# Kernel optimization log

Measured on AMD Instinct MI355X. Metric: run time of the kernel, lower is better.

## Reference

```python
import jax, jax.numpy as jnp
import numpy as np

N = 65536      # voxels
NFIX = 4096    # fixed-BC voxels (x == 0)
H = 128        # MLP hidden width
NFORCE = 4096  # force-surface points
E0 = 1.0
NU = 0.3
PENAL = 3.0
EM_V = 1e-3    # element volume
L_FIX = 0.05   # BC ramp length for analytical fixed-BC scale
K_FIX = E0 * 100.0
NUM_HUTCH = 50


def mlp(params, x):
    W1, b1, W2, b2, W3, b3, W4, b4 = params
    h = jnp.tanh(x @ W1 + b1)
    h = jnp.tanh(h @ W2 + b2)
    h = jnp.tanh(h @ W3 + b3)
    return h @ W4 + b4


def bc_scale(coord):
    # analytical fixed-BC scale: 0 exactly on the fixed face (x==0), ramps to 1
    return jnp.clip(coord[..., 0] / L_FIX, 0.0, 1.0)


def hutchinson_trace(params, coords, key, num_samples=NUM_HUTCH):
    # tr(J J^T) estimate via v^T J J^T v = ||J^T v||^2, batched VJPs (replaces
    # the per-sample autograd.grad python loop).
    out, vjp_fn = jax.vjp(lambda p: mlp(p, coords), params)

    def step(acc, k):
        v = jax.random.normal(k, out.shape, dtype=out.dtype)
        (g,) = vjp_fn(v)
        flat = jnp.concatenate([x.reshape(-1) for x in jax.tree_util.tree_leaves(g)])
        return acc + flat @ flat, None

    keys = jax.random.split(key, num_samples)
    tot, _ = jax.lax.scan(step, jnp.float32(0.0), keys)
    return tot / num_samples


def setup_inputs() -> dict:
    key = jax.random.key(0)
    ks = jax.random.split(key, 12)
    coord = jax.random.uniform(ks[0], (N, 3), dtype=jnp.float32)
    coord = coord.at[:, 0].set(0.02 + 0.98 * coord[:, 0])  # free voxels: x > 0
    coord = coord.at[:NFIX, 0].set(0.0)                    # fixed voxels: x == 0
    xPhys_m = jax.random.uniform(ks[1], (N, 1), dtype=jnp.float32)
    def lin(k, fi, fo):
        return jax.random.normal(k, (fi, fo), dtype=jnp.float32) / jnp.sqrt(jnp.float32(fi))
    W1 = lin(ks[2], 3, H); b1 = jnp.zeros((H,), jnp.float32)
    W2 = lin(ks[3], H, H); b2 = jnp.zeros((H,), jnp.float32)
    W3 = lin(ks[4], H, H); b3 = jnp.zeros((H,), jnp.float32)
    W4 = lin(ks[5], H, 3); b4 = jnp.zeros((3,), jnp.float32)
    force_coords = jax.random.uniform(ks[6], (NFORCE, 3), dtype=jnp.float32)
    F_vector = jax.random.normal(ks[7], (3,), dtype=jnp.float32)
    return dict(xPhys_m=xPhys_m, coord=coord, W1=W1, b1=b1, W2=W2, b2=b2,
                W3=W3, b3=b3, W4=W4, b4=b4, force_coords=force_coords,
                F_vector=F_vector, n_fix=NFIX)


def reference(xPhys_m, coord, W1, b1, W2, b2, W3, b3, W4, b4,
              force_coords, F_vector, n_fix):
    params = (W1, b1, W2, b2, W3, b3, W4, b4)

    u = mlp(params, coord)                       # [N,3] displacements
    scale = bc_scale(coord)                      # [N]
    fixed_mask = (scale == 0.0)

    # fixed-BC penalty energy
    u_fix = u * fixed_mask[:, None].astype(u.dtype)
    E_fix_all = xPhys_m ** PENAL * 0.5 * K_FIX * jnp.sum(u_fix ** 2, axis=1, keepdims=True)
    n_fix_ratio = jnp.float32(n_fix) / jnp.float32(N)
    E_fix = jnp.mean(E_fix_all[:n_fix]) * n_fix_ratio * EM_V

    # NTK-based adaptive weight via Hutchinson trace (detached, like .item())
    hkey = jax.random.key(42)
    ku, kr = jax.random.split(hkey)
    tr_uu = hutchinson_trace(params, coord[:n_fix], ku)
    tr_rr = hutchinson_trace(params, coord[n_fix:], kr)
    lam_fix = jax.lax.stop_gradient(jnp.clip(tr_rr / (tr_uu + 1e-12), 1e-3, 1e3))

    # per-voxel displacement Jacobian J[n, i, j] = d u_i / d coord_j  (batched
    # fwd-mode replaces three autograd.grad calls)
    J = jax.vmap(jax.jacfwd(lambda c: mlp(params, c)))(coord)  # [N,3,3]
    ux = J[:, 1, :]   # grads of u[:,1] (u0 in source)
    uy = J[:, 0, :]   # grads of u[:,0] (u1 in source)
    uz = J[:, 2, :]
    eps11 = ux[:, 1]
    eps12 = 0.5 * ux[:, 0] + 0.5 * uy[:, 1]
    eps13 = 0.5 * ux[:, 2] + 0.5 * uz[:, 1]
    eps22 = uy[:, 0]
    eps23 = 0.5 * uy[:, 2] + 0.5 * uz[:, 0]
    eps33 = uz[:, 2]

    lame_mu = E0 / (2.0 * (1.0 + NU))
    lame_lambda = E0 * NU / ((1.0 + NU) * (1.0 - 2.0 * NU))
    tr_strain = eps11 + eps22 + eps33
    sq_diag = eps11 * eps11 + eps22 * eps22 + eps33 * eps33
    energy = (0.5 * lame_lambda * tr_strain * tr_strain
              + lame_mu * (sq_diag + 2.0 * (eps12 * eps12 + eps13 * eps13 + eps23 * eps23)))
    energy = energy[:, None] * xPhys_m ** PENAL   # [N,1]
    energy_c = energy * 2.0
    energy_ans = EM_V * jnp.mean(energy)

    force_l = jnp.sum(mlp(params, force_coords) @ F_vector)

    loss = energy_ans - force_l + lam_fix * E_fix
    return (loss, energy_c, u)
```

## Files before the change

### kernel.cpp

```cpp
#include <hip/hip_runtime.h>
#include <math.h>

typedef __bf16 bf16x8 __attribute__((ext_vector_type(8)));
typedef __bf16 bf16x4 __attribute__((ext_vector_type(4)));
typedef float f32x4 __attribute__((ext_vector_type(4)));

#define HDIM 128
#define NTHREADS 512

#define EMV 0.001f
#define LFIX 0.05f
#define KFIX 100.0f
#define LAMBDA_L 0.5769230769230769f
#define MU_L 0.3846153846153846f

__device__ __forceinline__ int swb(int r, int blk) {
    return (r << 7) + ((blk ^ (r & 7)) << 3);
}
__device__ __forceinline__ int swb32(int r, int g) {
    return (r << 5) + ((g ^ ((r >> 1) & 3)) << 3);
}

__device__ __forceinline__ float fast_tanh(float x) {
    float xc = fminf(fmaxf(x, -10.f), 10.f);
    float e = __expf(2.f * xc);
    return 1.f - 2.f * __builtin_amdgcn_rcpf(e + 1.f);
}

__device__ __forceinline__ float wred(float v) {
#pragma unroll
    for (int off = 32; off > 0; off >>= 1) v += __shfl_down(v, off, 64);
    return v;
}

template <int NB, int CT0, int CT1>
__device__ __forceinline__ void gemm_f8(const bf16x8 (&aw)[4],
                                        __bf16* const* inb, __bf16* const* outb,
                                        const float* __restrict__ bsL,
                                        int wid, int l15, int q) {
    f32x4 acc[NB][CT1 - CT0];
#pragma unroll
    for (int b = 0; b < NB; ++b)
#pragma unroll
        for (int c = 0; c < CT1 - CT0; ++c) acc[b][c] = (f32x4){0.f, 0.f, 0.f, 0.f};

#pragma unroll
    for (int s = 0; s < 4; ++s)
#pragma unroll
        for (int b = 0; b < NB; ++b)
#pragma unroll
            for (int c = CT0; c < CT1; ++c) {
                bf16x8 bfr = *(const bf16x8*)(inb[b] + swb(c * 16 + l15, s * 4 + q));
                acc[b][c - CT0] = __builtin_amdgcn_mfma_f32_16x16x32_bf16(
                    aw[s], bfr, acc[b][c - CT0], 0, 0, 0);
            }
    __syncthreads();
    const int n0 = wid * 16 + q * 4;
    float4 bv = *(const float4*)(bsL + n0);
    float bias4[4] = {bv.x, bv.y, bv.z, bv.w};
#pragma unroll
    for (int c = CT0; c < CT1; ++c) {
        const int p = c * 16 + l15;
        const int widx = swb(p, n0 >> 3) + (n0 & 7);
        bf16x4 hv;
        float fct[4];
#pragma unroll
        for (int i = 0; i < 4; ++i) {
            float h = fast_tanh(acc[0][c - CT0][i] + bias4[i]);
            hv[i] = (__bf16)h;
            fct[i] = 1.f - h * h;
        }
        *(bf16x4*)(outb[0] + widx) = hv;
#pragma unroll
        for (int b = 1; b < NB; ++b) {
            bf16x4 ov;
#pragma unroll
            for (int i = 0; i < 4; ++i) ov[i] = (__bf16)(acc[b][c - CT0][i] * fct[i]);
            *(bf16x4*)(outb[b] + widx) = ov;
        }
    }
}

template <int NB>
__device__ __forceinline__ void gemm_tr8(const float* __restrict__ Wg, __bf16* Wst,
                                         __bf16* const* bufs,
                                         const __bf16* __restrict__ href,
                                         int wid, int l15, int q, int tid) {
    f32x4 acc[NB][2];
#pragma unroll
    for (int b = 0; b < NB; ++b) {
        acc[b][0] = (f32x4){0.f, 0.f, 0.f, 0.f};
        acc[b][1] = (f32x4){0.f, 0.f, 0.f, 0.f};
    }
#pragma unroll
    for (int c = 0; c < 4; ++c) {
        __syncthreads();
        {
            int j = tid >> 2, k8 = tid & 3;
            const float4* src = (const float4*)(Wg + j * HDIM + c * 32 + k8 * 8);
            float4 v0 = src[0], v1 = src[1];
            bf16x8 pk = {(__bf16)v0.x, (__bf16)v0.y, (__bf16)v0.z, (__bf16)v0.w,
                         (__bf16)v1.x, (__bf16)v1.y, (__bf16)v1.z, (__bf16)v1.w};
            *(bf16x8*)(Wst + swb32(j, k8)) = pk;
        }
        __syncthreads();
        bf16x8 afr = *(const bf16x8*)(Wst + swb32(wid * 16 + l15, q));
#pragma unroll
        for (int b = 0; b < NB; ++b) {
            bf16x8 b0 = *(const bf16x8*)(bufs[b] + swb(l15, c * 4 + q));
            acc[b][0] = __builtin_amdgcn_mfma_f32_16x16x32_bf16(afr, b0, acc[b][0], 0, 0, 0);
            bf16x8 b1 = *(const bf16x8*)(bufs[b] + swb(16 + l15, c * 4 + q));
            acc[b][1] = __builtin_amdgcn_mfma_f32_16x16x32_bf16(afr, b1, acc[b][1], 0, 0, 0);
        }
    }
    __syncthreads();
    const int n0 = wid * 16 + q * 4;
#pragma unroll
    for (int ct = 0; ct < 2; ++ct) {
        const int p = ct * 16 + l15;
        const int widx = swb(p, n0 >> 3) + (n0 & 7);
        bf16x4 hv = *(const bf16x4*)(href + widx);
        float fct[4];
#pragma unroll
        for (int i = 0; i < 4; ++i) {
            float h = (float)hv[i];
            fct[i] = 1.f - h * h;
        }
#pragma unroll
        for (int b = 0; b < NB; ++b) {
            bf16x4 ov;
#pragma unroll
            for (int i = 0; i < 4; ++i) ov[i] = (__bf16)(acc[b][ct][i] * fct[i]);
            *(bf16x4*)(bufs[b] + widx) = ov;
        }
    }
}

__device__ __forceinline__ void dnorms8(const __bf16* a, const __bf16* b, const __bf16* c2,
                                        float* npart, int tid) {
    int p = tid & 31, cc = tid >> 5;
    bf16x8 v0 = *(const bf16x8*)(a + swb(p, cc));
    bf16x8 v1 = *(const bf16x8*)(b + swb(p, cc));
    bf16x8 v2 = *(const bf16x8*)(c2 + swb(p, cc));
    float s0 = 0.f, s1 = 0.f, s2 = 0.f;
#pragma unroll
    for (int e = 0; e < 8; ++e) {
        float f0 = (float)v0[e], f1 = (float)v1[e], f2 = (float)v2[e];
        s0 += f0 * f0;
        s1 += f1 * f1;
        s2 += f2 * f2;
    }
    npart[(0 + cc) * 32 + p] = s0;
    npart[(16 + cc) * 32 + p] = s1;
    npart[(32 + cc) * 32 + p] = s2;
}

__device__ __forceinline__ float sum16(const float* npart, int buf, int p) {
    float d = 0.f;
#pragma unroll
    for (int i = 0; i < 16; ++i) d += npart[(buf * 16 + i) * 32 + p];
    return d;
}
__device__ __forceinline__ float sum48(const float* npart, int p) {
    float d = 0.f;
#pragma unroll
    for (int i = 0; i < 48; ++i) d += npart[i * 32 + p];
    return d;
}

__global__ void __launch_bounds__(NTHREADS, 4) pinn_all(
    const float* __restrict__ xPhys, const float* __restrict__ coord,
    const float* __restrict__ W1, const float* __restrict__ b1,
    const float* __restrict__ W2, const float* __restrict__ b2,
    const float* __restrict__ W3, const float* __restrict__ b3,
    const float* __restrict__ W4, const float* __restrict__ b4,
    const float* __restrict__ fc, const float* __restrict__ Fv,
    const int* __restrict__ nfixp,
    float* __restrict__ energy_c_out, float* __restrict__ u_out,
    float* __restrict__ acc, int nm32, int nmain64, int ntrb, int NF) {
    __shared__ __align__(16) __bf16 pool[32768];
    __shared__ __align__(16) __bf16 W4p[16 * HDIM];
    __shared__ __align__(16) float W1s[4 * HDIM];
    __shared__ __align__(16) float W4ts[3 * HDIM];
    __shared__ __align__(16) float gls[64 * 12];
    __shared__ __align__(16) float uls[64 * 4];
    __shared__ float nh1s[32], nh2s[32], nh3s[32];

    const int tid = threadIdx.x;
    const int lane = tid & 63, wid = tid >> 6, l15 = lane & 15, q = lane >> 4;
    const int bi = blockIdx.x;
    const int nfixv = nfixp[0];

    int ttile = -1;
    if (bi < ntrb) {
        const int nfull = nfixv >> 5;
        const int cm = (nfixv & 31) ? 1 : 0;
        const int c1 = (nfull + 7) >> 3;
        int t;
        if (bi < c1) {
            t = bi << 3;
        } else if (cm && bi == c1) {
            t = nfull;
        } else {
            const int rr0 = nfull + cm;
            const int f0 = rr0 + ((8 - (rr0 & 15) + 16) & 15);
            t = f0 + ((bi - c1 - cm) << 4);
        }
        if (t >= nm32) return;
        ttile = t;
    }

    for (int i = tid; i < 3 * HDIM; i += NTHREADS) W1s[i] = W1[i];
    if (tid < HDIM) W1s[3 * HDIM + tid] = b1[tid];
    if (tid < 3 * HDIM) W4ts[tid] = W4[(tid & 127) * 3 + (tid >> 7)];
    if (tid < 256) {
        int o = tid >> 4, blk = tid & 15, j0 = blk * 8;
        bf16x8 pk;
#pragma unroll
        for (int e = 0; e < 8; ++e) pk[e] = (__bf16)((o < 3) ? W4[(j0 + e) * 3 + o] : 0.f);
        *(bf16x8*)(W4p + swb(o, blk)) = pk;
    }
    bf16x8 aw2[4], aw3[4];
#pragma unroll
    for (int s = 0; s < 4; ++s) {
        const int kb = s * 32 + q * 8;
        const int n = wid * 16 + l15;
        bf16x8 v2, v3;
#pragma unroll
        for (int e = 0; e < 8; ++e) {
            v2[e] = (__bf16)W2[(kb + e) * HDIM + n];
            v3[e] = (__bf16)W3[(kb + e) * HDIM + n];
        }
        aw2[s] = v2;
        aw3[s] = v3;
    }
    __syncthreads();

    if (bi < ntrb) {
        const int base = ttile * 32;
        __bf16* H1 = pool;
        __bf16* H2 = pool + 4096;
        __bf16* H3 = pool + 8192;
        __bf16* T0 = pool + 12288;
        __bf16* T1 = pool + 16384;
        __bf16* T2 = pool + 20480;
        __bf16* WST = pool + 24576;
        float* npart = (float*)(pool + 28672);

        {
            const int p = lane & 31, sub = lane >> 5;
            const int blk = wid * 2 + sub, j0 = blk * 8;
            const float* cp = coord + (base + p) * 3;
            float x0 = cp[0], x1 = cp[1], x2 = cp[2];
            bf16x8 hv, t0v, t1v, t2v;
#pragma unroll
            for (int jj = 0; jj < 8; ++jj) {
                int j = j0 + jj;
                float w0 = W1s[j], w1 = W1s[HDIM + j], w2 = W1s[2 * HDIM + j];
                float z = W1s[3 * HDIM + j] + x0 * w0 + x1 * w1 + x2 * w2;
                float h = fast_tanh(z);
                float fct = 1.f - h * h;
                hv[jj] = (__bf16)h;
                t0v[jj] = (__bf16)(fct * w0);
                t1v[jj] = (__bf16)(fct * w1);
                t2v[jj] = (__bf16)(fct * w2);
            }
            int wi = swb(p, blk);
            *(bf16x8*)(H1 + wi) = hv;
            *(bf16x8*)(T0 + wi) = t0v;
            *(bf16x8*)(T1 + wi) = t1v;
            *(bf16x8*)(T2 + wi) = t2v;
        }
        __syncthreads();
        {
            __bf16* ib[4] = {H1, T0, T1, T2};
            __bf16* ob[4] = {H2, T0, T1, T2};
            gemm_f8<4, 0, 2>(aw2, ib, ob, b2, wid, l15, q);
        }
        __syncthreads();
        {
            __bf16* ib[4] = {H2, T0, T1, T2};
            __bf16* ob[4] = {H3, T0, T1, T2};
            gemm_f8<4, 0, 2>(aw3, ib, ob, b3, wid, l15, q);
        }
        __syncthreads();

        dnorms8(H1, H2, H3, npart, tid);
        __syncthreads();
        if (tid < 32) {
            nh1s[tid] = sum16(npart, 0, tid);
            nh2s[tid] = sum16(npart, 1, tid);
            nh3s[tid] = sum16(npart, 2, tid);
        }
        __syncthreads();
        {
            const int p = lane & 31, sub = lane >> 5;
            const int blk = wid * 2 + sub, j0 = blk * 8;
            bf16x8 h3v = *(const bf16x8*)(H3 + swb(p, blk));
            bf16x8 d0, d1, d2;
#pragma unroll
            for (int e = 0; e < 8; ++e) {
                float h = (float)h3v[e];
                float fct = 1.f - h * h;
                d0[e] = (__bf16)(fct * W4ts[j0 + e]);
                d1[e] = (__bf16)(fct * W4ts[HDIM + j0 + e]);
                d2[e] = (__bf16)(fct * W4ts[2 * HDIM + j0 + e]);
            }
            int wi = swb(p, blk);
            *(bf16x8*)(T0 + wi) = d0;
            *(bf16x8*)(T1 + wi) = d1;
            *(bf16x8*)(T2 + wi) = d2;
        }
        __syncthreads();
        float s_acc = 0.f;
        dnorms8(T0, T1, T2, npart, tid);
        __syncthreads();
        if (tid < 32) s_acc = sum48(npart, tid) * (1.f + nh2s[tid]);
        {
            __bf16* ib[3] = {T0, T1, T2};
            gemm_tr8<3>(W3, WST, ib, H2, wid, l15, q, tid);
        }
        __syncthreads();
        dnorms8(T0, T1, T2, npart, tid);
        __syncthreads();
        if (tid < 32) s_acc += sum48(npart, tid) * (1.f + nh1s[tid]);
        {
            __bf16* ib[3] = {T0, T1, T2};
            gemm_tr8<3>(W2, WST, ib, H1, wid, l15, q, tid);
        }
        __syncthreads();
        dnorms8(T0, T1, T2, npart, tid);
        __syncthreads();
        if (tid < 64) {
            float su = 0.f, sr = 0.f, cu = 0.f, cr = 0.f;
            if (tid < 32) {
                int p = tid;
                const float* cp = coord + (base + p) * 3;
                float x0 = cp[0], x1 = cp[1], x2 = cp[2];
                float nx = x0 * x0 + x1 * x1 + x2 * x2;
                float s = s_acc + sum48(npart, p) * (1.f + nx) + 3.f * (nh3s[p] + 1.f);
                bool uu = (base + p) < nfixv;
                su = uu ? s : 0.f;
                sr = uu ? 0.f : s;
                cu = uu ? 1.f : 0.f;
                cr = uu ? 0.f : 1.f;
            }
            su = wred(su);
            sr = wred(sr);
            cu = wred(cu);
            cr = wred(cr);
            if (tid == 0) {
                atomicAdd(acc + 3, su);
                atomicAdd(acc + 4, sr);
                atomicAdd(acc + 5, cu);
                atomicAdd(acc + 6, cr);
            }
        }
    } else if (bi < ntrb + nmain64) {
        const int base = (bi - ntrb) * 64;
        __bf16* HF = pool;
        __bf16* TF0 = pool + 8192;
        __bf16* TF1 = pool + 16384;
        __bf16* TF2 = pool + 24576;

        {
            const int p = lane;
            const float* cp = coord + (base + p) * 3;
            float x0 = cp[0], x1 = cp[1], x2 = cp[2];
#pragma unroll
            for (int it2 = 0; it2 < 2; ++it2) {
                const int blk = it2 * 8 + wid, j0 = blk * 8;
                bf16x8 hv, t0v, t1v, t2v;
#pragma unroll
                for (int jj = 0; jj < 8; ++jj) {
                    int j = j0 + jj;
                    float w0 = W1s[j], w1 = W1s[HDIM + j], w2 = W1s[2 * HDIM + j];
                    float z = W1s[3 * HDIM + j] + x0 * w0 + x1 * w1 + x2 * w2;
                    float h = fast_tanh(z);
                    float fct = 1.f - h * h;
                    hv[jj] = (__bf16)h;
                    t0v[jj] = (__bf16)(fct * w0);
                    t1v[jj] = (__bf16)(fct * w1);
                    t2v[jj] = (__bf16)(fct * w2);
                }
                int wi = swb(p, blk);
                *(bf16x8*)(HF + wi) = hv;
                *(bf16x8*)(TF0 + wi) = t0v;
                *(bf16x8*)(TF1 + wi) = t1v;
                *(bf16x8*)(TF2 + wi) = t2v;
            }
        }
        __syncthreads();
        {
            __bf16* ib[4] = {HF, TF0, TF1, TF2};
            gemm_f8<4, 0, 2>(aw2, ib, ib, b2, wid, l15, q);
            gemm_f8<4, 2, 4>(aw2, ib, ib, b2, wid, l15, q);
        }
        __syncthreads();
        {
            __bf16* ib[4] = {HF, TF0, TF1, TF2};
            gemm_f8<4, 0, 2>(aw3, ib, ib, b3, wid, l15, q);
            gemm_f8<4, 2, 4>(aw3, ib, ib, b3, wid, l15, q);
        }
        __syncthreads();

        {
            f32x4 ha0 = (f32x4){0.f, 0.f, 0.f, 0.f};
            f32x4 ha1 = (f32x4){0.f, 0.f, 0.f, 0.f};
            if (wid < 4) {
                const int ct = wid;
#pragma unroll
                for (int s = 0; s < 4; ++s) {
                    int kb = s * 4 + q;
                    bf16x8 af = *(const bf16x8*)(W4p + swb(l15, kb));
                    bf16x8 bA = *(const bf16x8*)(HF + swb(ct * 16 + l15, kb));
                    ha0 = __builtin_amdgcn_mfma_f32_16x16x32_bf16(af, bA, ha0, 0, 0, 0);
                    bf16x8 bB = *(const bf16x8*)(TF0 + swb(ct * 16 + l15, kb));
                    ha1 = __builtin_amdgcn_mfma_f32_16x16x32_bf16(af, bB, ha1, 0, 0, 0);
                }
                if (q == 0) {
                    int p = ct * 16 + l15;
#pragma unroll
                    for (int o = 0; o < 3; ++o) {
                        float uv = ha0[o] + b4[o];
                        uls[p * 4 + o] = uv;
                        u_out[(base + p) * 3 + o] = uv;
                    }
#pragma unroll
                    for (int o = 0; o < 3; ++o) gls[p * 12 + o] = ha1[o];
                }
            } else {
                const int ct = wid - 4;
#pragma unroll
                for (int s = 0; s < 4; ++s) {
                    int kb = s * 4 + q;
                    bf16x8 af = *(const bf16x8*)(W4p + swb(l15, kb));
                    bf16x8 bA = *(const bf16x8*)(TF1 + swb(ct * 16 + l15, kb));
                    ha0 = __builtin_amdgcn_mfma_f32_16x16x32_bf16(af, bA, ha0, 0, 0, 0);
                    bf16x8 bB = *(const bf16x8*)(TF2 + swb(ct * 16 + l15, kb));
                    ha1 = __builtin_amdgcn_mfma_f32_16x16x32_bf16(af, bB, ha1, 0, 0, 0);
                }
                if (q == 0) {
                    int p = ct * 16 + l15;
#pragma unroll
                    for (int o = 0; o < 3; ++o) gls[p * 12 + 3 + o] = ha0[o];
#pragma unroll
                    for (int o = 0; o < 3; ++o) gls[p * 12 + 6 + o] = ha1[o];
                }
            }
        }
        __syncthreads();

        if (tid < 64) {
            int p = tid;
            float x0 = coord[(base + p) * 3];
            float xp = xPhys[base + p];
            float xp3 = xp * xp * xp;
            float sc = fminf(fmaxf(x0 * (1.f / LFIX), 0.f), 1.f);
            float ef = 0.f;
            if ((base + p) < nfixv && sc == 0.f) {
                float u0 = uls[p * 4], u1 = uls[p * 4 + 1], u2 = uls[p * 4 + 2];
                ef = xp3 * 0.5f * KFIX * (u0 * u0 + u1 * u1 + u2 * u2);
            }
            float g00 = gls[p * 12 + 0], g01 = gls[p * 12 + 1], g02 = gls[p * 12 + 2];
            float g10 = gls[p * 12 + 3], g11 = gls[p * 12 + 4], g12 = gls[p * 12 + 5];
            float g20 = gls[p * 12 + 6], g21 = gls[p * 12 + 7], g22 = gls[p * 12 + 8];
            float e11 = g11, e22 = g00, e33 = g22;
            float e12 = 0.5f * (g01 + g10);
            float e13 = 0.5f * (g21 + g12);
            float e23 = 0.5f * (g20 + g02);
            float tr = e11 + e22 + e33;
            float en = 0.5f * LAMBDA_L * tr * tr +
                       MU_L * (e11 * e11 + e22 * e22 + e33 * e33 +
                               2.f * (e12 * e12 + e13 * e13 + e23 * e23));
            float exp3 = en * xp3;
            energy_c_out[base + p] = 2.f * exp3;
            float er = exp3;
            ef = wred(ef);
            er = wred(er);
            if (tid == 0) {
                atomicAdd(acc + 1, ef);
                atomicAdd(acc + 0, er);
            }
        }
    } else {
        const int fbase = (bi - ntrb - nmain64) * 64;
        __bf16* HF = pool;
        {
            int pp = fbase + lane;
            if (pp >= NF) pp = NF - 1;
            const float* cp = fc + pp * 3;
            float x0 = cp[0], x1 = cp[1], x2 = cp[2];
#pragma unroll
            for (int it2 = 0; it2 < 2; ++it2) {
                const int blk = it2 * 8 + wid, j0 = blk * 8;
                bf16x8 hv;
#pragma unroll
                for (int jj = 0; jj < 8; ++jj) {
                    int j = j0 + jj;
                    float z = W1s[3 * HDIM + j] + x0 * W1s[j] + x1 * W1s[HDIM + j] +
                              x2 * W1s[2 * HDIM + j];
                    hv[jj] = (__bf16)fast_tanh(z);
                }
                *(bf16x8*)(HF + swb(lane, blk)) = hv;
            }
        }
        __syncthreads();
        {
            __bf16* ib[1] = {HF};
            gemm_f8<1, 0, 2>(aw2, ib, ib, b2, wid, l15, q);
            gemm_f8<1, 2, 4>(aw2, ib, ib, b2, wid, l15, q);
        }
        __syncthreads();
        {
            __bf16* ib[1] = {HF};
            gemm_f8<1, 0, 2>(aw3, ib, ib, b3, wid, l15, q);
            gemm_f8<1, 2, 4>(aw3, ib, ib, b3, wid, l15, q);
        }
        __syncthreads();
        if (wid < 4) {
            const int ct = wid;
            f32x4 ha = (f32x4){0.f, 0.f, 0.f, 0.f};
#pragma unroll
            for (int s = 0; s < 4; ++s) {
                int kb = s * 4 + q;
                bf16x8 af = *(const bf16x8*)(W4p + swb(l15, kb));
                bf16x8 bf_ = *(const bf16x8*)(HF + swb(ct * 16 + l15, kb));
                ha = __builtin_amdgcn_mfma_f32_16x16x32_bf16(af, bf_, ha, 0, 0, 0);
            }
            if (q == 0) {
                int p = ct * 16 + l15;
#pragma unroll
                for (int o = 0; o < 3; ++o) uls[p * 4 + o] = ha[o] + b4[o];
            }
        }
        __syncthreads();
        if (tid < 64) {
            float fsum = 0.f;
            if (fbase + tid < NF)
                fsum = uls[tid * 4] * Fv[0] + uls[tid * 4 + 1] * Fv[1] +
                       uls[tid * 4 + 2] * Fv[2];
            fsum = wred(fsum);
            if (tid == 0) atomicAdd(acc + 2, fsum);
        }
    }
}

__global__ void pinn_final(const float* __restrict__ acc, float* __restrict__ out,
                           int Ntot, const int* __restrict__ nfixp) {
    float es = acc[0], ef = acc[1], fl = acc[2];
    float su = acc[3], sr = acc[4], cu = acc[5], cr = acc[6];
    float nfix = (float)nfixp[0];
    float tu = su / fmaxf(cu, 1.f) * nfix;
    float tr = sr / fmaxf(cr, 1.f) * ((float)Ntot - nfix);
    float energy_ans = EMV * (es / (float)Ntot);
    float E_fix = ef * EMV / (float)Ntot;
    float lam = tr / (tu + 1e-12f);
    lam = fminf(fmaxf(lam, 0.001f), 1000.f);
    out[0] = energy_ans - fl + lam * E_fix;
}

extern "C" void kernel_launch(void* const* d_in, const int* in_sizes, int n_in,
                              void* d_out, int out_size, void* d_ws, size_t ws_size,
                              hipStream_t stream) {
    const float* xPhys = (const float*)d_in[0];
    const float* coord = (const float*)d_in[1];
    const float* W1 = (const float*)d_in[2];
    const float* b1 = (const float*)d_in[3];
    const float* W2 = (const float*)d_in[4];
    const float* b2 = (const float*)d_in[5];
    const float* W3 = (const float*)d_in[6];
    const float* b3 = (const float*)d_in[7];
    const float* W4 = (const float*)d_in[8];
    const float* b4 = (const float*)d_in[9];
    const float* fc = (const float*)d_in[10];
    const float* Fv = (const float*)d_in[11];
    const int* nfix = (const int*)d_in[12];

    const int N = in_sizes[0];
    const int NF = in_sizes[10] / 3;
    float* out = (float*)d_out;
    float* acc = (float*)d_ws;

    const int nm32 = N / 32;
    const int nmain64 = N / 64;
    const int ntrb = nm32 / 8 + 2;
    const int nforce64 = (NF + 63) / 64;
    const int nblocks = ntrb + nmain64 + nforce64;
    (void)hipMemsetAsync(acc, 0, 8 * sizeof(float), stream);
    pinn_all<<<dim3(nblocks), dim3(NTHREADS), 0, stream>>>(
        xPhys, coord, W1, b1, W2, b2, W3, b3, W4, b4, fc, Fv, nfix,
        out + 1, out + 1 + N, acc, nm32, nmain64, ntrb, NF);
    pinn_final<<<dim3(1), dim3(1), 0, stream>>>(acc, out, N, nfix);
}
```

Measured before the change: 139.1 us.

## Fuse final reduction via last-block atomic counter, prefetch coords, drop tanh clamp

Removes the separate single-thread finalization kernel. The last block to finish, found through an atomic done-counter, now computes the scalar loss. Point coordinates are loaded at block start, before the weight staging, so their global-memory latency overlaps that work. The clamp inside fast_tanh is dropped; this relies on __expf overflowing to inf and rcp returning 0 to give saturation. Idle blocks no longer return early, because every block must take part in the counter. The change saves one launch at the cost of a threadfence in every block.

```diff
diff --git a/kernel.cpp b/kernel.cpp
--- a/kernel.cpp
+++ b/kernel.cpp
@@ -22,8 +22,7 @@
 }
 
 __device__ __forceinline__ float fast_tanh(float x) {
-    float xc = fminf(fmaxf(x, -10.f), 10.f);
-    float e = __expf(2.f * xc);
+    float e = __expf(2.f * x);
     return 1.f - 2.f * __builtin_amdgcn_rcpf(e + 1.f);
 }
 
@@ -177,7 +176,8 @@
     const float* __restrict__ fc, const float* __restrict__ Fv,
     const int* __restrict__ nfixp,
     float* __restrict__ energy_c_out, float* __restrict__ u_out,
-    float* __restrict__ acc, int nm32, int nmain64, int ntrb, int NF) {
+    float* __restrict__ acc, int nm32, int nmain64, int ntrb, int NF,
+    float* __restrict__ loss_out, int Ntot) {
     __shared__ __align__(16) __bf16 pool[32768];
     __shared__ __align__(16) __bf16 W4p[16 * HDIM];
     __shared__ __align__(16) float W1s[4 * HDIM];
@@ -192,6 +192,7 @@
     const int nfixv = nfixp[0];
 
     int ttile = -1;
+    bool idle = false;
     if (bi < ntrb) {
         const int nfull = nfixv >> 5;
         const int cm = (nfixv & 31) ? 1 : 0;
@@ -206,176 +207,71 @@
             const int f0 = rr0 + ((8 - (rr0 & 15) + 16) & 15);
             t = f0 + ((bi - c1 - cm) << 4);
         }
-        if (t >= nm32) return;
-        ttile = t;
-    }
-
-    for (int i = tid; i < 3 * HDIM; i += NTHREADS) W1s[i] = W1[i];
-    if (tid < HDIM) W1s[3 * HDIM + tid] = b1[tid];
-    if (tid < 3 * HDIM) W4ts[tid] = W4[(tid & 127) * 3 + (tid >> 7)];
-    if (tid < 256) {
-        int o = tid >> 4, blk = tid & 15, j0 = blk * 8;
-        bf16x8 pk;
-#pragma unroll
-        for (int e = 0; e < 8; ++e) pk[e] = (__bf16)((o < 3) ? W4[(j0 + e) * 3 + o] : 0.f);
-        *(bf16x8*)(W4p + swb(o, blk)) = pk;
-    }
-    bf16x8 aw2[4], aw3[4];
-#pragma unroll
-    for (int s = 0; s < 4; ++s) {
-        const int kb = s * 32 + q * 8;
-        const int n = wid * 16 + l15;
-        bf16x8 v2, v3;
-#pragma unroll
-        for (int e = 0; e < 8; ++e) {
-            v2[e] = (__bf16)W2[(kb + e) * HDIM + n];
-            v3[e] = (__bf16)W3[(kb + e) * HDIM + n];
-        }
-        aw2[s] = v2;
-        aw3[s] = v3;
-    }
-    __syncthreads();
-
-    if (bi < ntrb) {
-        const int base = ttile * 32;
-        __bf16* H1 = pool;
-        __bf16* H2 = pool + 4096;
-        __bf16* H3 = pool + 8192;
-        __bf16* T0 = pool + 12288;
-        __bf16* T1 = pool + 16384;
-        __bf16* T2 = pool + 20480;
-        __bf16* WST = pool + 24576;
-        float* npart = (float*)(pool + 28672);
-
-        {
-            const int p = lane & 31, sub = lane >> 5;
-            const int blk = wid * 2 + sub, j0 = blk * 8;
-            const float* cp = coord + (base + p) * 3;
-            float x0 = cp[0], x1 = cp[1], x2 = cp[2];
-            bf16x8 hv, t0v, t1v, t2v;
-#pragma unroll
-            for (int jj = 0; jj < 8; ++jj) {
-                int j = j0 + jj;
-                float w0 = W1s[j], w1 = W1s[HDIM + j], w2 = W1s[2 * HDIM + j];
-                float z = W1s[3 * HDIM + j] + x0 * w0 + x1 * w1 + x2 * w2;
-                float h = fast_tanh(z);
-                float fct = 1.f - h * h;
-                hv[jj] = (__bf16)h;
-                t0v[jj] = (__bf16)(fct * w0);
-                t1v[jj] = (__bf16)(fct * w1);
-                t2v[jj] = (__bf16)(fct * w2);
-            }
-            int wi = swb(p, blk);
-            *(bf16x8*)(H1 + wi) = hv;
-            *(bf16x8*)(T0 + wi) = t0v;
-            *(bf16x8*)(T1 + wi) = t1v;
-            *(bf16x8*)(T2 + wi) = t2v;
+        if (t >= nm32) idle = true;
+        else ttile = t;
+    }
+
+    if (!idle) {
+        float px0, px1, px2;
+        if (bi < ntrb) {
+            const float* cp = coord + (ttile * 32 + (lane & 31)) * 3;
+            px0 = cp[0]; px1 = cp[1]; px2 = cp[2];
+        } else if (bi < ntrb + nmain64) {
+            const float* cp = coord + ((bi - ntrb) * 64 + lane) * 3;
+            px0 = cp[0]; px1 = cp[1]; px2 = cp[2];
+        } else {
+            int pp = (bi - ntrb - nmain64) * 64 + lane;
+            if (pp >= NF) pp = NF - 1;
+            const float* cp = fc + pp * 3;
+            px0 = cp[0]; px1 = cp[1]; px2 = cp[2];
+        }
+
+        for (int i = tid; i < 3 * HDIM; i += NTHREADS) W1s[i] = W1[i];
+        if (tid < HDIM) W1s[3 * HDIM + tid] = b1[tid];
+        if (tid < 3 * HDIM) W4ts[tid] = W4[(tid & 127) * 3 + (tid >> 7)];
+        if (tid < 256) {
+            int o = tid >> 4, blk = tid & 15, j0 = blk * 8;
+            bf16x8 pk;
+#pragma unroll
+            for (int e = 0; e < 8; ++e) pk[e] = (__bf16)((o < 3) ? W4[(j0 + e) * 3 + o] : 0.f);
+            *(bf16x8*)(W4p + swb(o, blk)) = pk;
+        }
+        bf16x8 aw2[4], aw3[4];
+#pragma unroll
+        for (int s = 0; s < 4; ++s) {
+            const int kb = s * 32 + q * 8;
+            const int n = wid * 16 + l15;
+            bf16x8 v2, v3;
+#pragma unroll
+            for (int e = 0; e < 8; ++e) {
+                v2[e] = (__bf16)W2[(kb + e) * HDIM + n];
+                v3[e] = (__bf16)W3[(kb + e) * HDIM + n];
+            }
+            aw2[s] = v2;
+            aw3[s] = v3;
         }
         __syncthreads();
-        {
-            __bf16* ib[4] = {H1, T0, T1, T2};
-            __bf16* ob[4] = {H2, T0, T1, T2};
-            gemm_f8<4, 0, 2>(aw2, ib, ob, b2, wid, l15, q);
-        }
-        __syncthreads();
-        {
-            __bf16* ib[4] = {H2, T0, T1, T2};
-            __bf16* ob[4] = {H3, T0, T1, T2};
-            gemm_f8<4, 0, 2>(aw3, ib, ob, b3, wid, l15, q);
-        }
-        __syncthreads();
-
-        dnorms8(H1, H2, H3, npart, tid);
-        __syncthreads();
-        if (tid < 32) {
-            nh1s[tid] = sum16(npart, 0, tid);
-            nh2s[tid] = sum16(npart, 1, tid);
-            nh3s[tid] = sum16(npart, 2, tid);
-        }
-        __syncthreads();
-        {
-            const int p = lane & 31, sub = lane >> 5;
-            const int blk = wid * 2 + sub, j0 = blk * 8;
-            bf16x8 h3v = *(const bf16x8*)(H3 + swb(p, blk));
-            bf16x8 d0, d1, d2;
-#pragma unroll
-            for (int e = 0; e < 8; ++e) {
-                float h = (float)h3v[e];
-                float fct = 1.f - h * h;
-                d0[e] = (__bf16)(fct * W4ts[j0 + e]);
-                d1[e] = (__bf16)(fct * W4ts[HDIM + j0 + e]);
-                d2[e] = (__bf16)(fct * W4ts[2 * HDIM + j0 + e]);
-            }
-            int wi = swb(p, blk);
-            *(bf16x8*)(T0 + wi) = d0;
-            *(bf16x8*)(T1 + wi) = d1;
-            *(bf16x8*)(T2 + wi) = d2;
-        }
-        __syncthreads();
-        float s_acc = 0.f;
-        dnorms8(T0, T1, T2, npart, tid);
-        __syncthreads();
-        if (tid < 32) s_acc = sum48(npart, tid) * (1.f + nh2s[tid]);
-        {
-            __bf16* ib[3] = {T0, T1, T2};
-            gemm_tr8<3>(W3, WST, ib, H2, wid, l15, q, tid);
-        }
-        __syncthreads();
-        dnorms8(T0, T1, T2, npart, tid);
-        __syncthreads();
-        if (tid < 32) s_acc += sum48(npart, tid) * (1.f + nh1s[tid]);
-        {
-            __bf16* ib[3] = {T0, T1, T2};
-            gemm_tr8<3>(W2, WST, ib, H1, wid, l15, q, tid);
-        }
-        __syncthreads();
-        dnorms8(T0, T1, T2, npart, tid);
-        __syncthreads();
-        if (tid < 64) {
-            float su = 0.f, sr = 0.f, cu = 0.f, cr = 0.f;
-            if (tid < 32) {
-                int p = tid;
-                const float* cp = coord + (base + p) * 3;
-                float x0 = cp[0], x1 = cp[1], x2 = cp[2];
-                float nx = x0 * x0 + x1 * x1 + x2 * x2;
-                float s = s_acc + sum48(npart, p) * (1.f + nx) + 3.f * (nh3s[p] + 1.f);
-                bool uu = (base + p) < nfixv;
-                su = uu ? s : 0.f;
-                sr = uu ? 0.f : s;
-                cu = uu ? 1.f : 0.f;
-                cr = uu ? 0.f : 1.f;
-            }
-            su = wred(su);
-            sr = wred(sr);
-            cu = wred(cu);
-            cr = wred(cr);
-            if (tid == 0) {
-                atomicAdd(acc + 3, su);
-                atomicAdd(acc + 4, sr);
-                atomicAdd(acc + 5, cu);
-                atomicAdd(acc + 6, cr);
-            }
-        }
-    } else if (bi < ntrb + nmain64) {
-        const int base = (bi - ntrb) * 64;
-        __bf16* HF = pool;
-        __bf16* TF0 = pool + 8192;
-        __bf16* TF1 = pool + 16384;
-        __bf16* TF2 = pool + 24576;
-
-        {
-            const int p = lane;
-            const float* cp = coord + (base + p) * 3;
-            float x0 = cp[0], x1 = cp[1], x2 = cp[2];
-#pragma unroll
-            for (int it2 = 0; it2 < 2; ++it2) {
-                const int blk = it2 * 8 + wid, j0 = blk * 8;
+
+        if (bi < ntrb) {
+            const int base = ttile * 32;
+            __bf16* H1 = pool;
+            __bf16* H2 = pool + 4096;
+            __bf16* H3 = pool + 8192;
+            __bf16* T0 = pool + 12288;
+            __bf16* T1 = pool + 16384;
+            __bf16* T2 = pool + 20480;
+            __bf16* WST = pool + 24576;
+            float* npart = (float*)(pool + 28672);
+
+            {
+                const int p = lane & 31, sub = lane >> 5;
+                const int blk = wid * 2 + sub, j0 = blk * 8;
                 bf16x8 hv, t0v, t1v, t2v;
 #pragma unroll
                 for (int jj = 0; jj < 8; ++jj) {
                     int j = j0 + jj;
                     float w0 = W1s[j], w1 = W1s[HDIM + j], w2 = W1s[2 * HDIM + j];
-                    float z = W1s[3 * HDIM + j] + x0 * w0 + x1 * w1 + x2 * w2;
+                    float z = W1s[3 * HDIM + j] + px0 * w0 + px1 * w1 + px2 * w2;
                     float h = fast_tanh(z);
                     float fct = 1.f - h * h;
                     hv[jj] = (__bf16)h;
@@ -384,180 +280,300 @@
                     t2v[jj] = (__bf16)(fct * w2);
                 }
                 int wi = swb(p, blk);
-                *(bf16x8*)(HF + wi) = hv;
-                *(bf16x8*)(TF0 + wi) = t0v;
-                *(bf16x8*)(TF1 + wi) = t1v;
-                *(bf16x8*)(TF2 + wi) = t2v;
-            }
-        }
-        __syncthreads();
-        {
-            __bf16* ib[4] = {HF, TF0, TF1, TF2};
-            gemm_f8<4, 0, 2>(aw2, ib, ib, b2, wid, l15, q);
-            gemm_f8<4, 2, 4>(aw2, ib, ib, b2, wid, l15, q);
-        }
-        __syncthreads();
-        {
-            __bf16* ib[4] = {HF, TF0, TF1, TF2};
-            gemm_f8<4, 0, 2>(aw3, ib, ib, b3, wid, l15, q);
-            gemm_f8<4, 2, 4>(aw3, ib, ib, b3, wid, l15, q);
-        }
-        __syncthreads();
-
-        {
-            f32x4 ha0 = (f32x4){0.f, 0.f, 0.f, 0.f};
-            f32x4 ha1 = (f32x4){0.f, 0.f, 0.f, 0.f};
+                *(bf16x8*)(H1 + wi) = hv;
+                *(bf16x8*)(T0 + wi) = t0v;
+                *(bf16x8*)(T1 + wi) = t1v;
+                *(bf16x8*)(T2 + wi) = t2v;
+            }
+            __syncthreads();
+            {
+                __bf16* ib[4] = {H1, T0, T1, T2};
+                __bf16* ob[4] = {H2, T0, T1, T2};
+                gemm_f8<4, 0, 2>(aw2, ib, ob, b2, wid, l15, q);
+            }
+            __syncthreads();
+            {
+                __bf16* ib[4] = {H2, T0, T1, T2};
+                __bf16* ob[4] = {H3, T0, T1, T2};
+                gemm_f8<4, 0, 2>(aw3, ib, ob, b3, wid, l15, q);
+            }
+            __syncthreads();
+
+            dnorms8(H1, H2, H3, npart, tid);
+            __syncthreads();
+            if (tid < 32) {
+                nh1s[tid] = sum16(npart, 0, tid);
+                nh2s[tid] = sum16(npart, 1, tid);
+                nh3s[tid] = sum16(npart, 2, tid);
+            }
+            __syncthreads();
+            {
+                const int p = lane & 31, sub = lane >> 5;
+                const int blk = wid * 2 + sub, j0 = blk * 8;
+                bf16x8 h3v = *(const bf16x8*)(H3 + swb(p, blk));
+                bf16x8 d0, d1, d2;
+#pragma unroll
+                for (int e = 0; e < 8; ++e) {
+                    float h = (float)h3v[e];
+                    float fct = 1.f - h * h;
+                    d0[e] = (__bf16)(fct * W4ts[j0 + e]);
+                    d1[e] = (__bf16)(fct * W4ts[HDIM + j0 + e]);
+                    d2[e] = (__bf16)(fct * W4ts[2 * HDIM + j0 + e]);
+                }
+                int wi = swb(p, blk);
+                *(bf16x8*)(T0 + wi) = d0;
+                *(bf16x8*)(T1 + wi) = d1;
+                *(bf16x8*)(T2 + wi) = d2;
+            }
+            __syncthreads();
+            float s_acc = 0.f;
+            dnorms8(T0, T1, T2, npart, tid);
+            __syncthreads();
+            if (tid < 32) s_acc = sum48(npart, tid) * (1.f + nh2s[tid]);
+            {
+                __bf16* ib[3] = {T0, T1, T2};
+                gemm_tr8<3>(W3, WST, ib, H2, wid, l15, q, tid);
+            }
+            __syncthreads();
+            dnorms8(T0, T1, T2, npart, tid);
+            __syncthreads();
+            if (tid < 32) s_acc += sum48(npart, tid) * (1.f + nh1s[tid]);
+            {
+                __bf16* ib[3] = {T0, T1, T2};
+                gemm_tr8<3>(W2, WST, ib, H1, wid, l15, q, tid);
+            }
+            __syncthreads();
+            dnorms8(T0, T1, T2, npart, tid);
+            __syncthreads();
+            if (tid < 64) {
+                float su = 0.f, sr = 0.f, cu = 0.f, cr = 0.f;
+                if (tid < 32) {
+                    int p = tid;
+                    float nx = px0 * px0 + px1 * px1 + px2 * px2;
+                    float s = s_acc + sum48(npart, p) * (1.f + nx) + 3.f * (nh3s[p] + 1.f);
+                    bool uu = (base + p) < nfixv;
+                    su = uu ? s : 0.f;
+                    sr = uu ? 0.f : s;
+                    cu = uu ? 1.f : 0.f;
+                    cr = uu ? 0.f : 1.f;
+                }
+                su = wred(su);
+                sr = wred(sr);
+                cu = wred(cu);
+                cr = wred(cr);
+                if (tid == 0) {
+                    atomicAdd(acc + 3, su);
+                    atomicAdd(acc + 4, sr);
+                    atomicAdd(acc + 5, cu);
+                    atomicAdd(acc + 6, cr);
+                }
+            }
+        } else if (bi < ntrb + nmain64) {
+            const int base = (bi - ntrb) * 64;
+            __bf16* HF = pool;
+            __bf16* TF0 = pool + 8192;
+            __bf16* TF1 = pool + 16384;
+            __bf16* TF2 = pool + 24576;
+
+            {
+                const int p = lane;
+#pragma unroll
+                for (int it2 = 0; it2 < 2; ++it2) {
+                    const int blk = it2 * 8 + wid, j0 = blk * 8;
+                    bf16x8 hv, t0v, t1v, t2v;
+#pragma unroll
+                    for (int jj = 0; jj < 8; ++jj) {
+                        int j = j0 + jj;
+                        float w0 = W1s[j], w1 = W1s[HDIM + j], w2 = W1s[2 * HDIM + j];
+                        float z = W1s[3 * HDIM + j] + px0 * w0 + px1 * w1 + px2 * w2;
+                        float h = fast_tanh(z);
+                        float fct = 1.f - h * h;
+                        hv[jj] = (__bf16)h;
+                        t0v[jj] = (__bf16)(fct * w0);
+                        t1v[jj] = (__bf16)(fct * w1);
+                        t2v[jj] = (__bf16)(fct * w2);
+                    }
+                    int wi = swb(p, blk);
+                    *(bf16x8*)(HF + wi) = hv;
+                    *(bf16x8*)(TF0 + wi) = t0v;
+                    *(bf16x8*)(TF1 + wi) = t1v;
+                    *(bf16x8*)(TF2 + wi) = t2v;
+                }
+            }
+            __syncthreads();
+            {
+                __bf16* ib[4] = {HF, TF0, TF1, TF2};
+                gemm_f8<4, 0, 2>(aw2, ib, ib, b2, wid, l15, q);
+                gemm_f8<4, 2, 4>(aw2, ib, ib, b2, wid, l15, q);
+            }
+            __syncthreads();
+            {
+                __bf16* ib[4] = {HF, TF0, TF1, TF2};
+                gemm_f8<4, 0, 2>(aw3, ib, ib, b3, wid, l15, q);
+                gemm_f8<4, 2, 4>(aw3, ib, ib, b3, wid, l15, q);
+            }
+            __syncthreads();
+
+            {
+                f32x4 ha0 = (f32x4){0.f, 0.f, 0.f, 0.f};
+                f32x4 ha1 = (f32x4){0.f, 0.f, 0.f, 0.f};
+                if (wid < 4) {
+                    const int ct = wid;
+#pragma unroll
+                    for (int s = 0; s < 4; ++s) {
+                        int kb = s * 4 + q;
+                        bf16x8 af = *(const bf16x8*)(W4p + swb(l15, kb));
+                        bf16x8 bA = *(const bf16x8*)(HF + swb(ct * 16 + l15, kb));
+                        ha0 = __builtin_amdgcn_mfma_f32_16x16x32_bf16(af, bA, ha0, 0, 0, 0);
+                        bf16x8 bB = *(const bf16x8*)(TF0 + swb(ct * 16 + l15, kb));
+                        ha1 = __builtin_amdgcn_mfma_f32_16x16x32_bf16(af, bB, ha1, 0, 0, 0);
+                    }
+                    if (q == 0) {
+                        int p = ct * 16 + l15;
+#pragma unroll
+                        for (int o = 0; o < 3; ++o) {
+                            float uv = ha0[o] + b4[o];
+                            uls[p * 4 + o] = uv;
+                            u_out[(base + p) * 3 + o] = uv;
+                        }
+#pragma unroll
+                        for (int o = 0; o < 3; ++o) gls[p * 12 + o] = ha1[o];
+                    }
+                } else {
+                    const int ct = wid - 4;
+#pragma unroll
+                    for (int s = 0; s < 4; ++s) {
+                        int kb = s * 4 + q;
+                        bf16x8 af = *(const bf16x8*)(W4p + swb(l15, kb));
+                        bf16x8 bA = *(const bf16x8*)(TF1 + swb(ct * 16 + l15, kb));
+                        ha0 = __builtin_amdgcn_mfma_f32_16x16x32_bf16(af, bA, ha0, 0, 0, 0);
+                        bf16x8 bB = *(const bf16x8*)(TF2 + swb(ct * 16 + l15, kb));
+                        ha1 = __builtin_amdgcn_mfma_f32_16x16x32_bf16(af, bB, ha1, 0, 0, 0);
+                    }
+                    if (q == 0) {
+                        int p = ct * 16 + l15;
+#pragma unroll
+                        for (int o = 0; o < 3; ++o) gls[p * 12 + 3 + o] = ha0[o];
+#pragma unroll
+                        for (int o = 0; o < 3; ++o) gls[p * 12 + 6 + o] = ha1[o];
+                    }
+                }
+            }
+            __syncthreads();
+
+            if (tid < 64) {
+                int p = tid;
+                float xp = xPhys[base + p];
+                float xp3 = xp * xp * xp;
+                float sc = fminf(fmaxf(px0 * (1.f / LFIX), 0.f), 1.f);
+                float ef = 0.f;
+                if ((base + p) < nfixv && sc == 0.f) {
+                    float u0 = uls[p * 4], u1 = uls[p * 4 + 1], u2 = uls[p * 4 + 2];
+                    ef = xp3 * 0.5f * KFIX * (u0 * u0 + u1 * u1 + u2 * u2);
+                }
+                float g00 = gls[p * 12 + 0], g01 = gls[p * 12 + 1], g02 = gls[p * 12 + 2];
+                float g10 = gls[p * 12 + 3], g11 = gls[p * 12 + 4], g12 = gls[p * 12 + 5];
+                float g20 = gls[p * 12 + 6], g21 = gls[p * 12 + 7], g22 = gls[p * 12 + 8];
+                float e11 = g11, e22 = g00, e33 = g22;
+                float e12 = 0.5f * (g01 + g10);
+                float e13 = 0.5f * (g21 + g12);
+                float e23 = 0.5f * (g20 + g02);
+                float tr = e11 + e22 + e33;
+                float en = 0.5f * LAMBDA_L * tr * tr +
+                           MU_L * (e11 * e11 + e22 * e22 + e33 * e33 +
+                                   2.f * (e12 * e12 + e13 * e13 + e23 * e23));
+                float exp3 = en * xp3;
+                energy_c_out[base + p] = 2.f * exp3;
+                float er = exp3;
+                ef = wred(ef);
+                er = wred(er);
+                if (tid == 0) {
+                    atomicAdd(acc + 1, ef);
+                    atomicAdd(acc + 0, er);
+                }
+            }
+        } else {
+            const int fbase = (bi - ntrb - nmain64) * 64;
+            __bf16* HF = pool;
+            {
+#pragma unroll
+                for (int it2 = 0; it2 < 2; ++it2) {
+                    const int blk = it2 * 8 + wid, j0 = blk * 8;
+                    bf16x8 hv;
+#pragma unroll
+                    for (int jj = 0; jj < 8; ++jj) {
+                        int j = j0 + jj;
+                        float z = W1s[3 * HDIM + j] + px0 * W1s[j] + px1 * W1s[HDIM + j] +
+                                  px2 * W1s[2 * HDIM + j];
+                        hv[jj] = (__bf16)fast_tanh(z);
+                    }
+                    *(bf16x8*)(HF + swb(lane, blk)) = hv;
+                }
+            }
+            __syncthreads();
+            {
+                __bf16* ib[1] = {HF};
+                gemm_f8<1, 0, 2>(aw2, ib, ib, b2, wid, l15, q);
+                gemm_f8<1, 2, 4>(aw2, ib, ib, b2, wid, l15, q);
+            }
+            __syncthreads();
+            {
+                __bf16* ib[1] = {HF};
+                gemm_f8<1, 0, 2>(aw3, ib, ib, b3, wid, l15, q);
+                gemm_f8<1, 2, 4>(aw3, ib, ib, b3, wid, l15, q);
+            }
+            __syncthreads();
             if (wid < 4) {
                 const int ct = wid;
+                f32x4 ha = (f32x4){0.f, 0.f, 0.f, 0.f};
 #pragma unroll
                 for (int s = 0; s < 4; ++s) {
                     int kb = s * 4 + q;
                     bf16x8 af = *(const bf16x8*)(W4p + swb(l15, kb));
-                    bf16x8 bA = *(const bf16x8*)(HF + swb(ct * 16 + l15, kb));
-                    ha0 = __builtin_amdgcn_mfma_f32_16x16x32_bf16(af, bA, ha0, 0, 0, 0);
-                    bf16x8 bB = *(const bf16x8*)(TF0 + swb(ct * 16 + l15, kb));
-                    ha1 = __builtin_amdgcn_mfma_f32_16x16x32_bf16(af, bB, ha1, 0, 0, 0);
+                    bf16x8 bf_ = *(const bf16x8*)(HF + swb(ct * 16 + l15, kb));
+                    ha = __builtin_amdgcn_mfma_f32_16x16x32_bf16(af, bf_, ha, 0, 0, 0);
                 }
                 if (q == 0) {
                     int p = ct * 16 + l15;
 #pragma unroll
-                    for (int o = 0; o < 3; ++o) {
-                        float uv = ha0[o] + b4[o];
-                        uls[p * 4 + o] = uv;
-                        u_out[(base + p) * 3 + o] = uv;
-                    }
-#pragma unroll
-                    for (int o = 0; o < 3; ++o) gls[p * 12 + o] = ha1[o];
-                }
-            } else {
-                const int ct = wid - 4;
-#pragma unroll
-                for (int s = 0; s < 4; ++s) {
-                    int kb = s * 4 + q;
-                    bf16x8 af = *(const bf16x8*)(W4p + swb(l15, kb));
-                    bf16x8 bA = *(const bf16x8*)(TF1 + swb(ct * 16 + l15, kb));
-                    ha0 = __builtin_amdgcn_mfma_f32_16x16x32_bf16(af, bA, ha0, 0, 0, 0);
-                    bf16x8 bB = *(const bf16x8*)(TF2 + swb(ct * 16 + l15, kb));
-                    ha1 = __builtin_amdgcn_mfma_f32_16x16x32_bf16(af, bB, ha1, 0, 0, 0);
-                }
-                if (q == 0) {
-                    int p = ct * 16 + l15;
-#pragma unroll
-                    for (int o = 0; o < 3; ++o) gls[p * 12 + 3 + o] = ha0[o];
-#pragma unroll
-                    for (int o = 0; o < 3; ++o) gls[p * 12 + 6 + o] = ha1[o];
-                }
-            }
-        }
-        __syncthreads();
-
-        if (tid < 64) {
-            int p = tid;
-            float x0 = coord[(base + p) * 3];
-            float xp = xPhys[base + p];
-            float xp3 = xp * xp * xp;
-            float sc = fminf(fmaxf(x0 * (1.f / LFIX), 0.f), 1.f);
-            float ef = 0.f;
-            if ((base + p) < nfixv && sc == 0.f) {
-                float u0 = uls[p * 4], u1 = uls[p * 4 + 1], u2 = uls[p * 4 + 2];
-                ef = xp3 * 0.5f * KFIX * (u0 * u0 + u1 * u1 + u2 * u2);
-            }
-            float g00 = gls[p * 12 + 0], g01 = gls[p * 12 + 1], g02 = gls[p * 12 + 2];
-            float g10 = gls[p * 12 + 3], g11 = gls[p * 12 + 4], g12 = gls[p * 12 + 5];
-            float g20 = gls[p * 12 + 6], g21 = gls[p * 12 + 7], g22 = gls[p * 12 + 8];
-            float e11 = g11, e22 = g00, e33 = g22;
-            float e12 = 0.5f * (g01 + g10);
-            float e13 = 0.5f * (g21 + g12);
-            float e23 = 0.5f * (g20 + g02);
-            float tr = e11 + e22 + e33;
-            float en = 0.5f * LAMBDA_L * tr * tr +
-                       MU_L * (e11 * e11 + e22 * e22 + e33 * e33 +
-                               2.f * (e12 * e12 + e13 * e13 + e23 * e23));
-            float exp3 = en * xp3;
-            energy_c_out[base + p] = 2.f * exp3;
-            float er = exp3;
-            ef = wred(ef);
-            er = wred(er);
-            if (tid == 0) {
-                atomicAdd(acc + 1, ef);
-                atomicAdd(acc + 0, er);
-            }
-        }
-    } else {
-        const int fbase = (bi - ntrb - nmain64) * 64;
-        __bf16* HF = pool;
-        {
-            int pp = fbase + lane;
-            if (pp >= NF) pp = NF - 1;
-            const float* cp = fc + pp * 3;
-            float x0 = cp[0], x1 = cp[1], x2 = cp[2];
-#pragma unroll
-            for (int it2 = 0; it2 < 2; ++it2) {
-                const int blk = it2 * 8 + wid, j0 = blk * 8;
-                bf16x8 hv;
-#pragma unroll
-                for (int jj = 0; jj < 8; ++jj) {
-                    int j = j0 + jj;
-                    float z = W1s[3 * HDIM + j] + x0 * W1s[j] + x1 * W1s[HDIM + j] +
-                              x2 * W1s[2 * HDIM + j];
-                    hv[jj] = (__bf16)fast_tanh(z);
-                }
-                *(bf16x8*)(HF + swb(lane, blk)) = hv;
-            }
-        }
-        __syncthreads();
-        {
-            __bf16* ib[1] = {HF};
-            gemm_f8<1, 0, 2>(aw2, ib, ib, b2, wid, l15, q);
-            gemm_f8<1, 2, 4>(aw2, ib, ib, b2, wid, l15, q);
-        }
-        __syncthreads();
-        {
-            __bf16* ib[1] = {HF};
-            gemm_f8<1, 0, 2>(aw3, ib, ib, b3, wid, l15, q);
-            gemm_f8<1, 2, 4>(aw3, ib, ib, b3, wid, l15, q);
-        }
-        __syncthreads();
-        if (wid < 4) {
-            const int ct = wid;
-            f32x4 ha = (f32x4){0.f, 0.f, 0.f, 0.f};
-#pragma unroll
-            for (int s = 0; s < 4; ++s) {
-                int kb = s * 4 + q;
-                bf16x8 af = *(const bf16x8*)(W4p + swb(l15, kb));
-                bf16x8 bf_ = *(const bf16x8*)(HF + swb(ct * 16 + l15, kb));
-                ha = __builtin_amdgcn_mfma_f32_16x16x32_bf16(af, bf_, ha, 0, 0, 0);
-            }
-            if (q == 0) {
-                int p = ct * 16 + l15;
-#pragma unroll
-                for (int o = 0; o < 3; ++o) uls[p * 4 + o] = ha[o] + b4[o];
-            }
-        }
-        __syncthreads();
-        if (tid < 64) {
-            float fsum = 0.f;
-            if (fbase + tid < NF)
-                fsum = uls[tid * 4] * Fv[0] + uls[tid * 4 + 1] * Fv[1] +
-                       uls[tid * 4 + 2] * Fv[2];
-            fsum = wred(fsum);
-            if (tid == 0) atomicAdd(acc + 2, fsum);
-        }
-    }
-}
-
-__global__ void pinn_final(const float* __restrict__ acc, float* __restrict__ out,
-                           int Ntot, const int* __restrict__ nfixp) {
-    float es = acc[0], ef = acc[1], fl = acc[2];
-    float su = acc[3], sr = acc[4], cu = acc[5], cr = acc[6];
-    float nfix = (float)nfixp[0];
-    float tu = su / fmaxf(cu, 1.f) * nfix;
-    float tr = sr / fmaxf(cr, 1.f) * ((float)Ntot - nfix);
-    float energy_ans = EMV * (es / (float)Ntot);
-    float E_fix = ef * EMV / (float)Ntot;
-    float lam = tr / (tu + 1e-12f);
-    lam = fminf(fmaxf(lam, 0.001f), 1000.f);
-    out[0] = energy_ans - fl + lam * E_fix;
+                    for (int o = 0; o < 3; ++o) uls[p * 4 + o] = ha[o] + b4[o];
+                }
+            }
+            __syncthreads();
+            if (tid < 64) {
+                float fsum = 0.f;
+                if (fbase + tid < NF)
+                    fsum = uls[tid * 4] * Fv[0] + uls[tid * 4 + 1] * Fv[1] +
+                           uls[tid * 4 + 2] * Fv[2];
+                fsum = wred(fsum);
+                if (tid == 0) atomicAdd(acc + 2, fsum);
+            }
+        }
+    }
+
+    __threadfence();
+    if (tid == 0) {
+        unsigned* done = (unsigned*)(acc + 7);
+        unsigned old = atomicAdd(done, 1u);
+        if (old == (unsigned)gridDim.x - 1u) {
+            __threadfence();
+            float es = atomicAdd(acc + 0, 0.f);
+            float ef = atomicAdd(acc + 1, 0.f);
+            float fl = atomicAdd(acc + 2, 0.f);
+            float su = atomicAdd(acc + 3, 0.f);
+            float sr = atomicAdd(acc + 4, 0.f);
+            float cu = atomicAdd(acc + 5, 0.f);
+            float cr = atomicAdd(acc + 6, 0.f);
+            float nfix = (float)nfixv;
+            float tu = su / fmaxf(cu, 1.f) * nfix;
+            float tr = sr / fmaxf(cr, 1.f) * ((float)Ntot - nfix);
+            float energy_ans = EMV * (es / (float)Ntot);
+            float E_fix = ef * EMV / (float)Ntot;
+            float lam = tr / (tu + 1e-12f);
+            lam = fminf(fmaxf(lam, 0.001f), 1000.f);
+            loss_out[0] = energy_ans - fl + lam * E_fix;
+        }
+    }
 }
 
 extern "C" void kernel_launch(void* const* d_in, const int* in_sizes, int n_in,
@@ -590,6 +606,5 @@
     (void)hipMemsetAsync(acc, 0, 8 * sizeof(float), stream);
     pinn_all<<<dim3(nblocks), dim3(NTHREADS), 0, stream>>>(
         xPhys, coord, W1, b1, W2, b2, W3, b3, W4, b4, fc, Fv, nfix,
-        out + 1, out + 1 + N, acc, nm32, nmain64, ntrb, NF);
-    pinn_final<<<dim3(1), dim3(1), 0, stream>>>(acc, out, N, nfix);
-}
+        out + 1, out + 1 + N, acc, nm32, nmain64, ntrb, NF, out, N);
+}
```

After: 279.8 us. 101% more time.
